# Kernel optimization log

Measured on AMD Instinct MI355X. Metric: run time of the kernel, lower is better.

Reference implementation:

```python
import math
import jax, jax.numpy as jnp
import numpy as np

EMB = 1024
HEADS = 16
HEAD_DIM = EMB // HEADS
FF = 4 * EMB
EPS = 1e-5


def gelu_tanh(x):
    c = math.sqrt(2.0 / math.pi)
    return 0.5 * x * (1.0 + jnp.tanh(c * (x + 0.044715 * x ** 3)))


def layernorm(x, scale, shift):
    mean = jnp.mean(x, axis=-1, keepdims=True)
    var = jnp.var(x, axis=-1, keepdims=True)
    return scale * (x - mean) / jnp.sqrt(var + EPS) + shift


def setup_inputs() -> dict:
    key = jax.random.key(0)
    ks = jax.random.split(key, 10)
    s = 0.02
    return {
        "x": jax.random.normal(ks[0], (2, 2048, EMB), dtype=jnp.float32),
        "Wq": jax.random.normal(ks[1], (EMB, EMB), dtype=jnp.float32) * s,
        "Wk": jax.random.normal(ks[2], (EMB, EMB), dtype=jnp.float32) * s,
        "Wv": jax.random.normal(ks[3], (EMB, EMB), dtype=jnp.float32) * s,
        "Wo": jax.random.normal(ks[4], (EMB, EMB), dtype=jnp.float32) * s,
        "bo": jnp.zeros((EMB,), dtype=jnp.float32),
        "W1": jax.random.normal(ks[5], (EMB, FF), dtype=jnp.float32) * s,
        "b1": jnp.zeros((FF,), dtype=jnp.float32),
        "W2": jax.random.normal(ks[6], (FF, EMB), dtype=jnp.float32) * s,
        "b2": jnp.zeros((EMB,), dtype=jnp.float32),
        "ln1_scale": jnp.ones((EMB,), dtype=jnp.float32),
        "ln1_shift": jnp.zeros((EMB,), dtype=jnp.float32),
        "ln2_scale": jnp.ones((EMB,), dtype=jnp.float32),
        "ln2_shift": jnp.zeros((EMB,), dtype=jnp.float32),
    }


def reference(x, Wq, Wk, Wv, Wo, bo, W1, b1, W2, b2,
              ln1_scale, ln1_shift, ln2_scale, ln2_shift):
    B, S, D = x.shape
    # --- pre-LN causal MHA ---
    h = layernorm(x, ln1_scale, ln1_shift)
    q = (h @ Wq).reshape(B, S, HEADS, HEAD_DIM).transpose(0, 2, 1, 3)  # [B,H,S,d]
    k = (h @ Wk).reshape(B, S, HEADS, HEAD_DIM).transpose(0, 2, 1, 3)
    v = (h @ Wv).reshape(B, S, HEADS, HEAD_DIM).transpose(0, 2, 1, 3)
    scores = jnp.einsum("bhqd,bhkd->bhqk", q, k)  # [B,H,S,S]
    causal = jnp.triu(jnp.ones((S, S), dtype=bool), k=1)
    scores = jnp.where(causal, -jnp.inf, scores)
    attn = jax.nn.softmax(scores / math.sqrt(HEAD_DIM), axis=-1)
    ctx = jnp.einsum("bhqk,bhkd->bhqd", attn, v)  # [B,H,S,d]
    ctx = ctx.transpose(0, 2, 1, 3).reshape(B, S, D)
    x = x + (ctx @ Wo + bo)
    # --- FFN ---
    h = layernorm(x, ln2_scale, ln2_shift)
    h = gelu_tanh(h @ W1 + b1) @ W2 + b2
    return x + h
```

## Files before the change

### kernel.cpp

```cpp
#include <hip/hip_runtime.h>
#include <hip/hip_bf16.h>
#include <math.h>

#define EMB 1024
#define HEADS 16
#define HEAD_DIM 64
#define FF_DIM 4096
#define SEQ 2048
#define BATCH 2
#define NTOK (BATCH * SEQ)
#define LN_EPS 1e-5f
#define QKV_N 3072
#define Q_PRESCALE 0.18033688011112042f

typedef __attribute__((ext_vector_type(8))) short s8v;
typedef __attribute__((ext_vector_type(4))) float f4v;

__device__ __forceinline__ unsigned short f2bf(float f) {
    union { __hip_bfloat16 h; unsigned short u; } cv;
    cv.h = __float2bfloat16(f);
    return cv.u;
}

__device__ __forceinline__ float fast_exp2(float x) {
#if __has_builtin(__builtin_amdgcn_exp2f)
    return __builtin_amdgcn_exp2f(x);
#else
    return exp2f(x);
#endif
}

__device__ __forceinline__ float gelu_f(float x) {
    const float c = 0.7978845608028654f;
    float y = c * (x + 0.044715f * x * x * x);
    float e = fast_exp2(y * 2.8853900817779268f);
    float t = 1.0f - 2.0f / (e + 1.0f);
    return 0.5f * x * (1.0f + t);
}

#define GLDS(gp, lp)                                                        \
    __builtin_amdgcn_global_load_lds(                                       \
        (const __attribute__((address_space(1))) void*)(gp),                \
        (__attribute__((address_space(3))) void*)(lp), 16, 0, 0)

#define BAR()   do { __builtin_amdgcn_s_barrier(); __builtin_amdgcn_sched_barrier(0); } while (0)
#define LGKM0() do { asm volatile("s_waitcnt lgkmcnt(0)" ::: "memory"); __builtin_amdgcn_sched_barrier(0); } while (0)
#define VMCNT(n) do { asm volatile("s_waitcnt vmcnt(" #n ")" ::: "memory"); __builtin_amdgcn_sched_barrier(0); } while (0)

__global__ __launch_bounds__(256) void ln_bf16_kernel(const float* __restrict__ x,
                                                      const float* __restrict__ scale,
                                                      const float* __restrict__ shift,
                                                      unsigned short* __restrict__ out) {
    int row = blockIdx.x;
    int tid = threadIdx.x;
    const float4 xv = ((const float4*)(x + (size_t)row * EMB))[tid];
    float s  = xv.x + xv.y + xv.z + xv.w;
    float ss = xv.x * xv.x + xv.y * xv.y + xv.z * xv.z + xv.w * xv.w;
    __shared__ float2 red[256];
    red[tid] = make_float2(s, ss);
    __syncthreads();
    for (int off = 128; off > 0; off >>= 1) {
        if (tid < off) {
            red[tid].x += red[tid + off].x;
            red[tid].y += red[tid + off].y;
        }
        __syncthreads();
    }
    float mean = red[0].x * (1.0f / EMB);
    float var  = red[0].y * (1.0f / EMB) - mean * mean;
    float rstd = rsqrtf(var + LN_EPS);
    float4 sc4 = ((const float4*)scale)[tid];
    float4 sh4 = ((const float4*)shift)[tid];
    ushort4 o;
    o.x = f2bf(sc4.x * (xv.x - mean) * rstd + sh4.x);
    o.y = f2bf(sc4.y * (xv.y - mean) * rstd + sh4.y);
    o.z = f2bf(sc4.z * (xv.z - mean) * rstd + sh4.z);
    o.w = f2bf(sc4.w * (xv.w - mean) * rstd + sh4.w);
    *(ushort4*)(out + (size_t)row * EMB + tid * 4) = o;
}

__device__ __forceinline__ void tconv_tile(const float* __restrict__ W,
                                           unsigned short* __restrict__ Wt,
                                           int K, int N, int bx, int by, int tid) {
    __shared__ float t[64][65];
    int n0 = bx * 64, k0 = by * 64;
#pragma unroll
    for (int it = 0; it < 4; ++it) {
        int f = tid + it * 256;
        int r = f >> 4, c = (f & 15) * 4;
        float4 w = *(const float4*)(W + (size_t)(k0 + r) * N + n0 + c);
        t[r][c] = w.x; t[r][c + 1] = w.y; t[r][c + 2] = w.z; t[r][c + 3] = w.w;
    }
    __syncthreads();
#pragma unroll
    for (int it = 0; it < 4; ++it) {
        int f = tid + it * 256;
        int rn = f >> 4, ck = (f & 15) * 4;
        ushort4 o;
        o.x = f2bf(t[ck + 0][rn]);
        o.y = f2bf(t[ck + 1][rn]);
        o.z = f2bf(t[ck + 2][rn]);
        o.w = f2bf(t[ck + 3][rn]);
        *(ushort4*)(Wt + (size_t)(n0 + rn) * K + k0 + ck) = o;
    }
}

__global__ __launch_bounds__(256) void tconv_all_kernel(
    const float* __restrict__ Wq, const float* __restrict__ Wk,
    const float* __restrict__ Wv, const float* __restrict__ Wo,
    const float* __restrict__ W1, const float* __restrict__ W2,
    unsigned short* __restrict__ Wqkv_t, unsigned short* __restrict__ Wo_t,
    unsigned short* __restrict__ W1_t, unsigned short* __restrict__ W2_t) {
    int b = blockIdx.x;
    int tid = threadIdx.x;
    if (b < 256)        tconv_tile(Wq, Wqkv_t,                      EMB, EMB,    b & 15, b >> 4, tid);
    else if (b < 512)   tconv_tile(Wk, Wqkv_t + (size_t)1024 * EMB, EMB, EMB,    (b - 256) & 15, (b - 256) >> 4, tid);
    else if (b < 768)   tconv_tile(Wv, Wqkv_t + (size_t)2048 * EMB, EMB, EMB,    (b - 512) & 15, (b - 512) >> 4, tid);
    else if (b < 1024)  tconv_tile(Wo, Wo_t,                        EMB, EMB,    (b - 768) & 15, (b - 768) >> 4, tid);
    else if (b < 2048)  tconv_tile(W1, W1_t,                        EMB, FF_DIM, (b - 1024) & 63, (b - 1024) >> 6, tid);
    else                tconv_tile(W2, W2_t,                        FF_DIM, EMB, (b - 2048) & 15, (b - 2048) >> 4, tid);
}

__global__ __launch_bounds__(256) void reduce_kernel(const float* __restrict__ p0,
                                                     const float* __restrict__ p1,
                                                     const float* __restrict__ bias,
                                                     const float* __restrict__ residual,
                                                     float* __restrict__ out) {
    size_t i4 = ((size_t)blockIdx.x * 256 + threadIdx.x) * 4;
    float4 a = *(const float4*)(p0 + i4);
    float4 b = *(const float4*)(p1 + i4);
    float4 r = *(const float4*)(residual + i4);
    int col = (int)(i4 & (EMB - 1));
    float4 bs = *(const float4*)(bias + col);
    float4 o;
    o.x = a.x + b.x + r.x + bs.x;
    o.y = a.y + b.y + r.y + bs.y;
    o.z = a.z + b.z + r.z + bs.z;
    o.w = a.w + b.w + r.w + bs.w;
    *(float4*)(out + i4) = o;
}

__global__ __launch_bounds__(256) void reduce_ln_kernel(const float* __restrict__ p0,
                                                        const float* __restrict__ p1,
                                                        const float* __restrict__ bias,
                                                        const float* __restrict__ residual,
                                                        float* __restrict__ x1,
                                                        const float* __restrict__ scale,
                                                        const float* __restrict__ shift,
                                                        unsigned short* __restrict__ out) {
    int row = blockIdx.x;
    int tid = threadIdx.x;
    size_t i4 = (size_t)row * EMB + tid * 4;
    float4 a = *(const float4*)(p0 + i4);
    float4 b = *(const float4*)(p1 + i4);
    float4 r = *(const float4*)(residual + i4);
    float4 bs = *(const float4*)(bias + tid * 4);
    float4 xv;
    xv.x = a.x + b.x + r.x + bs.x;
    xv.y = a.y + b.y + r.y + bs.y;
    xv.z = a.z + b.z + r.z + bs.z;
    xv.w = a.w + b.w + r.w + bs.w;
    *(float4*)(x1 + i4) = xv;

    float s  = xv.x + xv.y + xv.z + xv.w;
    float ss = xv.x * xv.x + xv.y * xv.y + xv.z * xv.z + xv.w * xv.w;
    __shared__ float2 red[256];
    red[tid] = make_float2(s, ss);
    __syncthreads();
    for (int off = 128; off > 0; off >>= 1) {
        if (tid < off) {
            red[tid].x += red[tid + off].x;
            red[tid].y += red[tid + off].y;
        }
        __syncthreads();
    }
    float mean = red[0].x * (1.0f / EMB);
    float var  = red[0].y * (1.0f / EMB) - mean * mean;
    float rstd = rsqrtf(var + LN_EPS);
    float4 sc4 = ((const float4*)scale)[tid];
    float4 sh4 = ((const float4*)shift)[tid];
    ushort4 o;
    o.x = f2bf(sc4.x * (xv.x - mean) * rstd + sh4.x);
    o.y = f2bf(sc4.y * (xv.y - mean) * rstd + sh4.y);
    o.z = f2bf(sc4.z * (xv.z - mean) * rstd + sh4.z);
    o.w = f2bf(sc4.w * (xv.w - mean) * rstd + sh4.w);
    *(ushort4*)(out + i4) = o;
}

__global__ __launch_bounds__(256) void gemm_fused_kernel(
    const unsigned short* __restrict__ A,
    const unsigned short* __restrict__ Bt,
    unsigned short* __restrict__ Cb,
    int M, int N, int K,
    const float* __restrict__ bias,
    int do_gelu, int qkv_mode,
    unsigned short* __restrict__ vt)
{
    __shared__ short lds[24576];
    short* As = lds;
    short* Bs = lds + 12288;

    int tid = threadIdx.x;
    int nbx = N >> 7, nby8 = (M >> 7) >> 3;
    int bid = (int)blockIdx.x;
    int xcd = bid & 7;
    int t   = bid >> 3;
    int x   = t % nbx;
    int u   = t / nbx;
    int y   = (u % nby8) * 8 + xcd;
    int m0 = y << 7, n0 = x << 7;

    int wv = tid >> 6, lane = tid & 63;
    int wr = wv >> 1, wc = wv & 1;
    int quad = lane >> 4, ln = lane & 15;

    f4v acc[4][4];
#pragma unroll
    for (int i = 0; i < 4; ++i)
#pragma unroll
        for (int j = 0; j < 4; ++j) { f4v z4 = {0.f, 0.f, 0.f, 0.f}; acc[i][j] = z4; }

    int r0 = tid & 127;
    size_t Kby = (size_t)K << 1;
    const char* Ag0 = (const char*)A + (size_t)(m0 + r0) * Kby + (size_t)((tid >> 7) << 4);
    const char* Bg0 = (const char*)Bt + (size_t)(n0 + r0) * Kby + (size_t)((tid >> 7) << 4);

#define STAGE(tt, bi) do {                                                  \
    int kb_ = (tt) << 6;                                                    \
    char* Ad_ = (char*)As + (bi) * 8192 + tid * 16;                         \
    char* Bd_ = (char*)Bs + (bi) * 8192 + tid * 16;                         \
    GLDS(Ag0 + kb_, Ad_); GLDS(Ag0 + kb_ + 32, Ad_ + 4096);                 \
    GLDS(Bg0 + kb_, Bd_); GLDS(Bg0 + kb_ + 32, Bd_ + 4096); } while (0)

    int nIter = K >> 5;
    STAGE(0, 0);
    STAGE(1, 1);

    int cur = 0, stg = 2;
    for (int it = 0; it < nIter; ++it) {
        if (it + 1 < nIter) { VMCNT(4); } else { VMCNT(0); }
        BAR();
        if (it + 2 < nIter) {
            STAGE(it + 2, stg);
            __builtin_amdgcn_sched_barrier(0);
        }
        const short* Ab = As + cur * 4096;
        const short* Bb = Bs + cur * 4096;
        s8v af[4], bfr[4];
#pragma unroll
        for (int i = 0; i < 4; ++i)
            af[i] = *(const s8v*)(Ab + ((size_t)quad * 128 + wr * 64 + i * 16 + ln) * 8);
#pragma unroll
        for (int j = 0; j < 4; ++j)
            bfr[j] = *(const s8v*)(Bb + ((size_t)quad * 128 + wc * 64 + j * 16 + ln) * 8);
#pragma unroll
        for (int i = 0; i < 4; ++i)
#pragma unroll
            for (int j = 0; j < 4; ++j)
                acc[i][j] = __builtin_amdgcn_mfma_f32_16x16x32_bf16(af[i], bfr[j], acc[i][j], 0, 0, 0);
        cur = (cur == 2) ? 0 : cur + 1;
        stg = (stg == 2) ? 0 : stg + 1;
    }
#undef STAGE

    LGKM0();
    BAR();

    int colb = wc * 64 + ln;
    int rowb = wr * 64 + quad * 4;
    int off8 = (tid & 15) * 8;
    int sub  = tid >> 4;

    if (qkv_mode && n0 >= 2048) {
#pragma unroll
        for (int j = 0; j < 4; ++j) {
            int c = colb + j * 16;
            int swz = (c & 7) << 3;
#pragma unroll
            for (int i = 0; i < 4; ++i) {
                int rw = rowb + i * 16;
                ushort4 pk;
                pk.x = f2bf(acc[i][j][0]);
                pk.y = f2bf(acc[i][j][1]);
                pk.z = f2bf(acc[i][j][2]);
                pk.w = f2bf(acc[i][j][3]);
                *(ushort4*)(lds + c * 128 + (rw ^ swz)) = pk;
            }
        }
        BAR();
        int bb = m0 >> 11, s0b = m0 & 2047;
        size_t vbase = ((size_t)bb * 1024 + (n0 - 2048)) * SEQ + s0b + off8;
#pragma unroll
        for (int pass = 0; pass < 8; ++pass) {
            int c = pass * 16 + sub;
            s8v v = *(const s8v*)(lds + c * 128 + (off8 ^ ((c & 7) << 3)));
            *(s8v*)(vt + vbase + (size_t)c * SEQ) = v;
        }
        return;
    }

    bool isq = qkv_mode && (n0 < 1024);
#pragma unroll
    for (int j = 0; j < 4; ++j) {
        int c = colb + j * 16;
        float bj = (!qkv_mode && bias) ? bias[n0 + c] : 0.f;
#pragma unroll
        for (int i = 0; i < 4; ++i) {
            int rw = rowb + i * 16;
#pragma unroll
            for (int r = 0; r < 4; ++r) {
                float vv = acc[i][j][r];
                if (qkv_mode) { if (isq) vv *= Q_PRESCALE; }
                else { vv += bj; if (do_gelu) vv = gelu_f(vv); }
                int rr_ = rw + r;
                lds[rr_ * 128 + (c ^ ((rr_ & 7) << 3))] = (short)f2bf(vv);
            }
        }
    }
    BAR();
    int ldc = qkv_mode ? 2048 : N;
#pragma unroll
    for (int pass = 0; pass < 8; ++pass) {
        int rw = pass * 16 + sub;
        s8v v = *(const s8v*)(lds + rw * 128 + (off8 ^ ((rw & 7) << 3)));
        *(s8v*)(Cb + (size_t)(m0 + rw) * ldc + n0 + off8) = v;
    }
}

__global__ __launch_bounds__(256) void gemm_bf16_kernel(
    const unsigned short* __restrict__ A,
    const unsigned short* __restrict__ Bt,
    float* __restrict__ Cf0,
    float* __restrict__ Cf1,
    int M, int N, int K, int Klen)
{
    __shared__ short As[3][4096];
    __shared__ short Bs[3][4096];

    int tid = threadIdx.x;
    int nbx = N >> 7, nby8 = (M >> 7) >> 3;
    int bid = (int)blockIdx.x;
    int xcd = bid & 7;
    int t   = bid >> 3;
    int x   = t % nbx;
    int u   = t / nbx;
    int y   = (u % nby8) * 8 + xcd;
    int z   = u / nby8;

    int m0 = y << 7;
    int n0 = x << 7;
    int k0 = z * Klen;
    float* Cf = z ? Cf1 : Cf0;
    int wv = tid >> 6, lane = tid & 63;
    int wr = wv >> 1, wc = wv & 1;
    int quad = lane >> 4, ln = lane & 15;

    f4v acc[4][4];
#pragma unroll
    for (int i = 0; i < 4; ++i)
#pragma unroll
        for (int j = 0; j < 4; ++j) {
            f4v z4 = {0.f, 0.f, 0.f, 0.f};
            acc[i][j] = z4;
        }

    int r0 = tid & 127;
    size_t Kby = (size_t)K << 1;
    const char* Ag0 = (const char*)A + (size_t)(m0 + r0) * Kby + (size_t)k0 * 2 + (tid >> 7) * 16;
    const char* Bg0 = (const char*)Bt + (size_t)(n0 + r0) * Kby + (size_t)k0 * 2 + (tid >> 7) * 16;

#define STAGE(tt, bi) do {                                                  \
    int kb_ = (tt) << 6;                                                    \
    char* Ad_ = (char*)As[bi] + tid * 16;                                   \
    char* Bd_ = (char*)Bs[bi] + tid * 16;                                   \
    GLDS(Ag0 + kb_, Ad_); GLDS(Ag0 + kb_ + 32, Ad_ + 4096);                 \
    GLDS(Bg0 + kb_, Bd_); GLDS(Bg0 + kb_ + 32, Bd_ + 4096); } while (0)

    int nIter = Klen >> 5;
    STAGE(0, 0);
    STAGE(1, 1);

    int cur = 0, stg = 2;
    for (int it = 0; it < nIter; ++it) {
        if (it + 1 < nIter) { VMCNT(4); } else { VMCNT(0); }
        BAR();
        if (it + 2 < nIter) {
            STAGE(it + 2, stg);
            __builtin_amdgcn_sched_barrier(0);
        }
        const short* Ab = As[cur];
        const short* Bb = Bs[cur];
        s8v af[4], bfr[4];
#pragma unroll
        for (int i = 0; i < 4; ++i)
            af[i] = *(const s8v*)(Ab + ((size_t)quad * 128 + wr * 64 + i * 16 + ln) * 8);
#pragma unroll
        for (int j = 0; j < 4; ++j)
            bfr[j] = *(const s8v*)(Bb + ((size_t)quad * 128 + wc * 64 + j * 16 + ln) * 8);
#pragma unroll
        for (int i = 0; i < 4; ++i)
#pragma unroll
            for (int j = 0; j < 4; ++j)
                acc[i][j] = __builtin_amdgcn_mfma_f32_16x16x32_bf16(af[i], bfr[j], acc[i][j], 0, 0, 0);
        cur = (cur == 2) ? 0 : cur + 1;
        stg = (stg == 2) ? 0 : stg + 1;
    }
#undef STAGE

    int cn  = n0 + wc * 64 + ln;
    int cm0 = m0 + wr * 64 + quad * 4;
#pragma unroll
    for (int j = 0; j < 4; ++j) {
        int gn = cn + j * 16;
#pragma unroll
        for (int i = 0; i < 4; ++i)
#pragma unroll
            for (int r = 0; r < 4; ++r)
                Cf[(size_t)(cm0 + i * 16 + r) * N + gn] = acc[i][j][r];
    }
}

__global__ __launch_bounds__(256) void flash_attn_mfma_kernel(
    const unsigned short* __restrict__ qk,
    const unsigned short* __restrict__ vt,
    unsigned short* __restrict__ ctx)
{
    int h  = blockIdx.x;
    int b  = blockIdx.z;
    int qt = b ? (int)blockIdx.y : ((int)gridDim.y - 1 - (int)blockIdx.y);
    int tid = threadIdx.x;
    int w = tid >> 6, lane = tid & 63;
    int quad = lane >> 4, ln = lane & 15;

    __shared__ short Kb2[2][4096];
    __shared__ short Vb2[2][4096];
    __shared__ short Ps[4][32 * 72];

    size_t qrow0 = (size_t)b * SEQ + (size_t)qt * 128;
    int wrow0 = w * 32;

    s8v qf[2][2];
#pragma unroll
    for (int mb = 0; mb < 2; ++mb)
#pragma unroll
        for (int ks = 0; ks < 2; ++ks)
            qf[mb][ks] = *(const s8v*)(qk + (qrow0 + wrow0 + mb * 16 + ln) * 2048
                                          + h * 64 + ks * 32 + quad * 8);

    float l_part[2][4];
    f4v o[2][4];
#pragma unroll
    for (int mb = 0; mb < 2; ++mb) {
#pragma unroll
        for (int r = 0; r < 4; ++r) l_part[mb][r] = 0.f;
#pragma unroll
        for (int db = 0; db < 4; ++db) {
            f4v z = {0.f, 0.f, 0.f, 0.f};
            o[mb][db] = z;
        }
    }

    const unsigned short* kb_p = qk + (size_t)b * SEQ * 2048 + 1024 + h * 64;
    const unsigned short* vb_p = vt + ((size_t)b * 1024 + h * 64) * SEQ;
    short* Pw = Ps[w];

    int rr = tid & 63;
    const unsigned short* Kg0 = kb_p + (size_t)rr * 2048 + (tid >> 6) * 8;
    const unsigned short* Vg0 = vb_p + (size_t)rr * 2048 + (tid >> 6) * 8;

    int ktn = 2 * qt + 2;
    int ktmax_w = (qt * 128 + wrow0 + 31) >> 6;

    GLDS(Kg0, (char*)Kb2[0] + tid * 16);
    GLDS(Kg0 + 32, (char*)Kb2[0] + tid * 16 + 4096);
    GLDS(Vg0, (char*)Vb2[0] + tid * 16);
    GLDS(Vg0 + 32, (char*)Vb2[0] + tid * 16 + 4096);

    for (int kt = 0; kt < ktn; ++kt) {
        BAR();
        bool pf = (kt + 1 < ktn);
        if (pf) {
            int nb_ = (kt + 1) & 1;
            const unsigned short* ks_ = Kg0 + (size_t)(kt + 1) * 64 * 2048;
            const unsigned short* vs_ = Vg0 + (kt + 1) * 64;
            GLDS(ks_, (char*)Kb2[nb_] + tid * 16);
            GLDS(ks_ + 32, (char*)Kb2[nb_] + tid * 16 + 4096);
            GLDS(vs_, (char*)Vb2[nb_] + tid * 16);
            GLDS(vs_ + 32, (char*)Vb2[nb_] + tid * 16 + 4096);
        }
        if (kt > ktmax_w) continue;
        if (pf) { VMCNT(8); } else { VMCNT(0); }

        const short* Kl = Kb2[kt & 1];
        const short* Vl = Vb2[kt & 1];

        f4v s[2][4];
#pragma unroll
        for (int mb = 0; mb < 2; ++mb)
#pragma unroll
            for (int nb = 0; nb < 4; ++nb) {
                f4v z = {0.f, 0.f, 0.f, 0.f};
                s[mb][nb] = z;
            }
#pragma unroll
        for (int ks = 0; ks < 2; ++ks)
#pragma unroll
            for (int nb = 0; nb < 4; ++nb) {
                s8v kfr = *(const s8v*)(Kl + ((size_t)(ks * 4 + quad) * 64 + nb * 16 + ln) * 8);
#pragma unroll
                for (int mb = 0; mb < 2; ++mb)
                    s[mb][nb] = __builtin_amdgcn_mfma_f32_16x16x32_bf16(qf[mb][ks], kfr, s[mb][nb], 0, 0, 0);
            }

        bool edge = (kt == ktmax_w);
#pragma unroll
        for (int mb = 0; mb < 2; ++mb) {
#pragma unroll
            for (int r = 0; r < 4; ++r) {
                int rloc = mb * 16 + quad * 4 + r;
                float p[4];
                if (!edge) {
#pragma unroll
                    for (int nb = 0; nb < 4; ++nb)
                        p[nb] = fast_exp2(s[mb][nb][r]);
                } else {
                    int grow = qt * 128 + wrow0 + rloc;
#pragma unroll
                    for (int nb = 0; nb < 4; ++nb) {
                        int key = kt * 64 + nb * 16 + ln;
                        float e = fast_exp2(s[mb][nb][r]);
                        p[nb] = (key > grow) ? 0.f : e;
                    }
                }
                l_part[mb][r] += (p[0] + p[1]) + (p[2] + p[3]);
#pragma unroll
                for (int nb = 0; nb < 4; ++nb)
                    Pw[rloc * 72 + nb * 16 + ln] = f2bf(p[nb]);
            }
        }

#pragma unroll
        for (int ks = 0; ks < 2; ++ks) {
            s8v pf_[2];
#pragma unroll
            for (int mb = 0; mb < 2; ++mb)
                pf_[mb] = *(const s8v*)(Pw + (mb * 16 + ln) * 72 + ks * 32 + quad * 8);
#pragma unroll
            for (int db = 0; db < 4; ++db) {
                s8v vfr = *(const s8v*)(Vl + ((size_t)(ks * 4 + quad) * 64 + db * 16 + ln) * 8);
#pragma unroll
                for (int mb = 0; mb < 2; ++mb)
                    o[mb][db] = __builtin_amdgcn_mfma_f32_16x16x32_bf16(pf_[mb], vfr, o[mb][db], 0, 0, 0);
            }
        }
    }

    asm volatile("s_waitcnt vmcnt(0)" ::: "memory");

#pragma unroll
    for (int mb = 0; mb < 2; ++mb)
#pragma unroll
        for (int r = 0; r < 4; ++r) {
            float l = l_part[mb][r];
#pragma unroll
            for (int msk = 1; msk < 16; msk <<= 1)
                l += __shfl_xor(l, msk);
            float inv = 1.0f / l;
            size_t row = qrow0 + wrow0 + mb * 16 + quad * 4 + r;
#pragma unroll
            for (int db = 0; db < 4; ++db)
                ctx[row * EMB + h * 64 + db * 16 + ln] = f2bf(o[mb][db][r] * inv);
        }
}

extern "C" void kernel_launch(void* const* d_in, const int* in_sizes, int n_in,
                              void* d_out, int out_size, void* d_ws, size_t ws_size,
                              hipStream_t stream) {
    const float* x    = (const float*)d_in[0];
    const float* Wq   = (const float*)d_in[1];
    const float* Wk   = (const float*)d_in[2];
    const float* Wv   = (const float*)d_in[3];
    const float* Wo   = (const float*)d_in[4];
    const float* bo   = (const float*)d_in[5];
    const float* W1   = (const float*)d_in[6];
    const float* b1   = (const float*)d_in[7];
    const float* W2   = (const float*)d_in[8];
    const float* b2   = (const float*)d_in[9];
    const float* ln1s = (const float*)d_in[10];
    const float* ln1b = (const float*)d_in[11];
    const float* ln2s = (const float*)d_in[12];
    const float* ln2b = (const float*)d_in[13];
    float* out = (float*)d_out;

    const size_t MiB = 1024 * 1024;
    uint8_t* w8 = (uint8_t*)d_ws;
    unsigned short* Wqkv_t = (unsigned short*)(w8);
    unsigned short* Wo_t   = (unsigned short*)(w8 +  6 * MiB);
    unsigned short* W1_t   = (unsigned short*)(w8 +  8 * MiB);
    unsigned short* W2_t   = (unsigned short*)(w8 + 16 * MiB);
    unsigned short* act_bf = (unsigned short*)(w8 + 24 * MiB);
    unsigned short* qk_bf  = (unsigned short*)(w8 + 32 * MiB);
    unsigned short* vt     = (unsigned short*)(w8 + 48 * MiB);
    float*          p0a    = (float*)(w8 + 32 * MiB);
    float*          p1a    = (float*)(w8 + 48 * MiB);
    unsigned short* u_bf   = (unsigned short*)(w8 + 32 * MiB);
    float*          x1     = (float*)(w8 + 64 * MiB);
    float*          p0b    = (float*)(w8);
    float*          p1b    = (float*)(w8 + 80 * MiB);

    tconv_all_kernel<<<3072, 256, 0, stream>>>(Wq, Wk, Wv, Wo, W1, W2,
                                               Wqkv_t, Wo_t, W1_t, W2_t);

    ln_bf16_kernel<<<NTOK, 256, 0, stream>>>(x, ln1s, ln1b, act_bf);

    gemm_fused_kernel<<<(NTOK / 128) * (QKV_N / 128), 256, 0, stream>>>(
        act_bf, Wqkv_t, qk_bf, NTOK, QKV_N, EMB, nullptr, 0, 1, vt);

    flash_attn_mfma_kernel<<<dim3(HEADS, SEQ / 128, BATCH), 256, 0, stream>>>(qk_bf, vt, act_bf);

    gemm_bf16_kernel<<<(EMB / 128) * (NTOK / 128) * 2, 256, 0, stream>>>(
        act_bf, Wo_t, p0a, p1a, NTOK, EMB, EMB, 512);
    reduce_ln_kernel<<<NTOK, 256, 0, stream>>>(p0a, p1a, bo, x, x1, ln2s, ln2b, act_bf);

    gemm_fused_kernel<<<(NTOK / 128) * (FF_DIM / 128), 256, 0, stream>>>(
        act_bf, W1_t, u_bf, NTOK, FF_DIM, EMB, b1, 1, 0, nullptr);

    gemm_bf16_kernel<<<(EMB / 128) * (NTOK / 128) * 2, 256, 0, stream>>>(
        u_bf, W2_t, p0b, p1b, NTOK, EMB, FF_DIM, 2048);
    reduce_kernel<<<(NTOK * EMB) / 1024, 256, 0, stream>>>(p0b, p1b, b2, x1, out);
}
```

Baseline: 442.9 us.

## Load GEMM MFMA fragments directly from global memory, dropping LDS staging

Replaces the triple-buffered global-to-LDS staging pipeline in the fused GEMM with direct per-wave global loads of MFMA fragments into registers, double-buffered in registers across K steps. This removes the LDS traffic and the barrier on every iteration. In exchange each A/B tile row is fetched separately by two waves, which doubles global/L2 traffic, and each 16-byte load strides rows of K elements, so coalescing is poor and load latency is exposed. The LDS array is shrunk but kept, presumably for the epilogue.

```diff
diff --git a/kernel.cpp b/kernel.cpp
--- a/kernel.cpp
+++ b/kernel.cpp
@@ -196,9 +196,7 @@
     int do_gelu, int qkv_mode,
     unsigned short* __restrict__ vt)
 {
-    __shared__ short lds[24576];
-    short* As = lds;
-    short* Bs = lds + 12288;
+    __shared__ short lds[16384];
 
     int tid = threadIdx.x;
     int nbx = N >> 7, nby8 = (M >> 7) >> 3;
@@ -220,51 +218,31 @@
 #pragma unroll
         for (int j = 0; j < 4; ++j) { f4v z4 = {0.f, 0.f, 0.f, 0.f}; acc[i][j] = z4; }
 
-    int r0 = tid & 127;
-    size_t Kby = (size_t)K << 1;
-    const char* Ag0 = (const char*)A + (size_t)(m0 + r0) * Kby + (size_t)((tid >> 7) << 4);
-    const char* Bg0 = (const char*)Bt + (size_t)(n0 + r0) * Kby + (size_t)((tid >> 7) << 4);
-
-#define STAGE(tt, bi) do {                                                  \
-    int kb_ = (tt) << 6;                                                    \
-    char* Ad_ = (char*)As + (bi) * 8192 + tid * 16;                         \
-    char* Bd_ = (char*)Bs + (bi) * 8192 + tid * 16;                         \
-    GLDS(Ag0 + kb_, Ad_); GLDS(Ag0 + kb_ + 32, Ad_ + 4096);                 \
-    GLDS(Bg0 + kb_, Bd_); GLDS(Bg0 + kb_ + 32, Bd_ + 4096); } while (0)
+    const unsigned short* Ap = A + (size_t)(m0 + wr * 64 + ln) * K + quad * 8;
+    const unsigned short* Bp = Bt + (size_t)(n0 + wc * 64 + ln) * K + quad * 8;
+
+    s8v a0[4], b0[4], a1[4], b1[4];
+
+#define LOADF(da, db, koff) do {                                            \
+    _Pragma("unroll") for (int i_ = 0; i_ < 4; ++i_) {                      \
+        da[i_] = *(const s8v*)(Ap + (size_t)i_ * 16 * K + (koff));          \
+        db[i_] = *(const s8v*)(Bp + (size_t)i_ * 16 * K + (koff)); } } while (0)
+#define MFMA16(sa, sb) do {                                                 \
+    _Pragma("unroll") for (int i_ = 0; i_ < 4; ++i_)                        \
+    _Pragma("unroll") for (int j_ = 0; j_ < 4; ++j_)                        \
+        acc[i_][j_] = __builtin_amdgcn_mfma_f32_16x16x32_bf16(              \
+            sa[i_], sb[j_], acc[i_][j_], 0, 0, 0); } while (0)
 
     int nIter = K >> 5;
-    STAGE(0, 0);
-    STAGE(1, 1);
-
-    int cur = 0, stg = 2;
-    for (int it = 0; it < nIter; ++it) {
-        if (it + 1 < nIter) { VMCNT(4); } else { VMCNT(0); }
-        BAR();
-        if (it + 2 < nIter) {
-            STAGE(it + 2, stg);
-            __builtin_amdgcn_sched_barrier(0);
-        }
-        const short* Ab = As + cur * 4096;
-        const short* Bb = Bs + cur * 4096;
-        s8v af[4], bfr[4];
-#pragma unroll
-        for (int i = 0; i < 4; ++i)
-            af[i] = *(const s8v*)(Ab + ((size_t)quad * 128 + wr * 64 + i * 16 + ln) * 8);
-#pragma unroll
-        for (int j = 0; j < 4; ++j)
-            bfr[j] = *(const s8v*)(Bb + ((size_t)quad * 128 + wc * 64 + j * 16 + ln) * 8);
-#pragma unroll
-        for (int i = 0; i < 4; ++i)
-#pragma unroll
-            for (int j = 0; j < 4; ++j)
-                acc[i][j] = __builtin_amdgcn_mfma_f32_16x16x32_bf16(af[i], bfr[j], acc[i][j], 0, 0, 0);
-        cur = (cur == 2) ? 0 : cur + 1;
-        stg = (stg == 2) ? 0 : stg + 1;
-    }
-#undef STAGE
-
-    LGKM0();
-    BAR();
+    LOADF(a0, b0, 0);
+    for (int it = 0; it < nIter; it += 2) {
+        LOADF(a1, b1, (it + 1) * 32);
+        MFMA16(a0, b0);
+        if (it + 2 < nIter) LOADF(a0, b0, (it + 2) * 32);
+        MFMA16(a1, b1);
+    }
+#undef LOADF
+#undef MFMA16
 
     int colb = wc * 64 + ln;
     int rowb = wr * 64 + quad * 4;
```

Result: slower. 534.6 us (+20.7%).
